# Optimization experiments

Measured on AMD Instinct MI355X. Metric: run time of the kernel, lower is better.

Reference implementation:

```python
import jax, jax.numpy as jnp
import numpy as np

B, T, D = 8, 2048, 1024
H, C, DV = 8, 64, 128   # n_heads, latent_dim, d_head
LN_EPS = 1e-5
NORM_EPS = 1e-12  # F.normalize eps


def _xavier(k, shape, fan_in, fan_out):
    lim = float(np.sqrt(6.0 / (fan_in + fan_out)))
    return jax.random.uniform(k, shape, jnp.float32, -lim, lim)


def setup_inputs() -> dict:
    key = jax.random.key(0)
    ks = jax.random.split(key, 9)
    x = jax.random.normal(ks[0], (B, T, D), jnp.float32)
    Wq = _xavier(ks[1], (C, D), D, C)            # S_q weight (out,in)
    Wk = _xavier(ks[2], (C, D), D, C)            # S_k
    Wv = _xavier(ks[3], (C, D), D, C)            # S_v
    Qc = _xavier(ks[4], (H, C, C), C, C)         # per-head latent rotations
    Vc = _xavier(ks[5], (H, C, DV), C, DV)       # per-head value up-proj
    Wa_w = _xavier(ks[6], (H * C, D), D, H * C)  # W_alpha weight
    Wa_b = jnp.full((H * C,), 3.0, jnp.float32)  # W_alpha bias init = 3.0
    Wo = _xavier(ks[7], (D, H * DV), H * DV, D)  # output proj
    gamma = jnp.ones((D,), jnp.float32)
    beta = jnp.zeros((D,), jnp.float32)
    return {"x": x, "Wq": Wq, "Wk": Wk, "Wv": Wv, "Qc": Qc, "Vc": Vc,
            "Wa_w": Wa_w, "Wa_b": Wa_b, "Wo": Wo, "gamma": gamma, "beta": beta}


def _forward(x, Wq, Wk, Wv, Qc, Vc, Wa_w, Wa_b, Wo, gamma, beta):
    residual = x
    # LayerNorm (biased variance, like torch)
    mu = jnp.mean(x, axis=-1, keepdims=True)
    var = jnp.mean(jnp.square(x - mu), axis=-1, keepdims=True)
    xn = (x - mu) * jax.lax.rsqrt(var + LN_EPS) * gamma + beta

    q_lat = xn @ Wq.T          # (B,T,C)
    k_lat = xn @ Wk.T          # (B,T,C) shared across heads
    v_lat = xn @ Wv.T          # (B,T,C)

    q = jnp.einsum('btc,hce->bhte', q_lat, Qc)   # (B,H,T,C)
    v = jnp.einsum('btc,hcd->bhtd', v_lat, Vc)   # (B,H,T,DV)
    alpha = jax.nn.sigmoid(xn @ Wa_w.T + Wa_b)   # (B,T,H*C)
    alpha = alpha.reshape(x.shape[0], x.shape[1], H, C).transpose(0, 2, 1, 3)  # (B,H,T,C)

    # F.normalize(k, dim=-1): k / max(||k||, eps)
    kn = k_lat / jnp.maximum(jnp.linalg.norm(k_lat, axis=-1, keepdims=True), NORM_EPS)

    # time-major for scan
    qs = jnp.moveaxis(q, 2, 0)      # (T,B,H,C)
    vs = jnp.moveaxis(v, 2, 0)      # (T,B,H,DV)
    als = jnp.moveaxis(alpha, 2, 0)  # (T,B,H,C)
    kns = jnp.moveaxis(kn, 1, 0)    # (T,B,C)

    S0 = jnp.zeros((x.shape[0], H, C, DV), x.dtype)

    def step(S, inp):
        q_t, k_t, v_t, a_t = inp
        # S_t = diag(alpha_t) S_{t-1} + k_t v_t^T  (k shared across heads)
        S = a_t[..., None] * S + k_t[:, None, :, None] * v_t[..., None, :]
        o_t = jnp.einsum('bhcv,bhc->bhv', S, q_t)
        return S, o_t

    _, outs = jax.lax.scan(step, S0, (qs, kns, vs, als))  # outs: (T,B,H,DV)
    out = jnp.moveaxis(outs, 0, 1).reshape(x.shape[0], x.shape[1], H * DV)
    return out @ Wo.T + residual


def reference(x, Wq, Wk, Wv, Qc, Vc, Wa_w, Wa_b, Wo, gamma, beta):
    return _forward(x, Wq, Wk, Wv, Qc, Vc, Wa_w, Wa_b, Wo, gamma, beta)
```

## Files before the change

### kernel.cpp

```cpp
#include <hip/hip_runtime.h>

typedef unsigned short u16;
typedef unsigned int   u32;
typedef __bf16 bf16x8 __attribute__((ext_vector_type(8)));
typedef float  f32x4  __attribute__((ext_vector_type(4)));
typedef float  f32x16 __attribute__((ext_vector_type(16)));

#define B_  8
#define T_  2048
#define D_  1024
#define H_  8
#define C_  64
#define DV_ 128
#define M_  (B_*T_)
#define L_  128
#define NC_ (T_/L_)
#define TS_ 8

__device__ __forceinline__ u16 f2bf(float f){
  u32 u = __float_as_uint(f);
  u32 r = (u + 0x7fffu + ((u >> 16) & 1u)) >> 16;
  return (u16)r;
}
__device__ __forceinline__ float bf2f(u16 u){
  return __uint_as_float(((u32)u) << 16);
}

__global__ __launch_bounds__(256) void ln_kernel(
    const float* __restrict__ x, const float* __restrict__ gamma,
    const float* __restrict__ beta, u16* __restrict__ xnb){
  const int m = blockIdx.x;
  const int tid = threadIdx.x;
  const int wave = tid >> 6, lane = tid & 63;
  const float* xr = x + (size_t)m * D_;
  float4 xv = *(const float4*)&xr[tid*4];
  float s = xv.x + xv.y + xv.z + xv.w;
  #pragma unroll
  for (int off = 32; off > 0; off >>= 1) s += __shfl_xor(s, off, 64);
  __shared__ float red[8];
  if (lane == 0) red[wave] = s;
  __syncthreads();
  float mu = (red[0]+red[1]+red[2]+red[3]) * (1.f/1024.f);
  float dx = xv.x-mu, dy = xv.y-mu, dz = xv.z-mu, dw = xv.w-mu;
  float ss = dx*dx + dy*dy + dz*dz + dw*dw;
  #pragma unroll
  for (int off = 32; off > 0; off >>= 1) ss += __shfl_xor(ss, off, 64);
  if (lane == 0) red[4+wave] = ss;
  __syncthreads();
  float var = (red[4]+red[5]+red[6]+red[7]) * (1.f/1024.f);
  float rs = rsqrtf(var + 1e-5f);
  float4 g  = *(const float4*)&gamma[tid*4];
  float4 bb = *(const float4*)&beta[tid*4];
  ushort4 o4;
  o4.x = f2bf(dx*rs*g.x + bb.x);
  o4.y = f2bf(dy*rs*g.y + bb.y);
  o4.z = f2bf(dz*rs*g.z + bb.z);
  o4.w = f2bf(dw*rs*g.w + bb.w);
  *(ushort4*)&xnb[(size_t)m*D_ + tid*4] = o4;
}

__global__ __launch_bounds__(256) void prep_weights(
    const float* __restrict__ Wq, const float* __restrict__ Wk,
    const float* __restrict__ Wv, const float* __restrict__ Wa,
    const float* __restrict__ Qc, const float* __restrict__ Vc,
    const float* __restrict__ Wo,
    u16* __restrict__ Wcatb, u16* __restrict__ QcTb,
    u16* __restrict__ VcTb,  u16* __restrict__ Wob){
  int idx = blockIdx.x * 256 + threadIdx.x;
  if (idx < 720896){
    int r = idx >> 10, col = idx & 1023;
    float v;
    if (r < 64)       v = Wq[(size_t)r*1024 + col];
    else if (r < 128) v = Wk[(size_t)(r-64)*1024 + col];
    else if (r < 192) v = Wv[(size_t)(r-128)*1024 + col];
    else              v = Wa[(size_t)(r-192)*1024 + col];
    Wcatb[idx] = f2bf(v);
  } else if (idx < 753664){
    int i = idx - 720896;
    int n = i >> 6, c = i & 63; int h = n >> 6, e = n & 63;
    QcTb[i] = f2bf(Qc[((size_t)h*64 + c)*64 + e]);
  } else if (idx < 819200){
    int i = idx - 753664;
    int n = i >> 6, c = i & 63; int h = n >> 7, d = n & 127;
    VcTb[i] = f2bf(Vc[((size_t)h*64 + c)*128 + d]);
  } else if (idx < 1867776){
    int i = idx - 819200;
    Wob[i] = f2bf(Wo[i]);
  }
}

__global__ __launch_bounds__(256) void gemm_bf16(
    const u16* __restrict__ A, const u16* __restrict__ Bw,
    float* __restrict__ C, const float* __restrict__ res,
    u16* __restrict__ Cb, int N, int K){
  __shared__ u16 As[128][36];
  __shared__ u16 Bs[64][36];
  const int tid = threadIdx.x;
  const int wave = tid >> 6;
  const int lane = tid & 63;
  const int q  = lane >> 4;
  const int mr = lane & 15;
  const int m0 = blockIdx.x * 128;
  const int n0 = blockIdx.y * 64;

  union FragU { u32 u[4]; bf16x8 v; };
  f32x4 zero = {0.f, 0.f, 0.f, 0.f};
  f32x4 acc[2][4];
  #pragma unroll
  for (int i = 0; i < 2; i++)
    #pragma unroll
    for (int j = 0; j < 4; j++) acc[i][j] = zero;

  for (int k0 = 0; k0 < K; k0 += 32){
    #pragma unroll
    for (int p = 0; p < 2; ++p){
      int ch = p*256 + tid;
      int r = ch >> 2, c4 = ch & 3;
      const uint4 val = *(const uint4*)(&A[(size_t)(m0 + r)*K + k0 + c4*8]);
      u32* dst = (u32*)&As[r][c4*8];
      dst[0]=val.x; dst[1]=val.y; dst[2]=val.z; dst[3]=val.w;
    }
    {
      int r = tid >> 2, c4 = tid & 3;
      const uint4 val = *(const uint4*)(&Bw[(size_t)(n0 + r)*K + k0 + c4*8]);
      u32* dst = (u32*)&Bs[r][c4*8];
      dst[0]=val.x; dst[1]=val.y; dst[2]=val.z; dst[3]=val.w;
    }
    __syncthreads();
    bf16x8 afr[2], bfr[4];
    #pragma unroll
    for (int mt = 0; mt < 2; mt++){
      const u32* p = (const u32*)&As[wave*32 + mt*16 + mr][q*8];
      FragU f; f.u[0]=p[0]; f.u[1]=p[1]; f.u[2]=p[2]; f.u[3]=p[3];
      afr[mt] = f.v;
    }
    #pragma unroll
    for (int nt = 0; nt < 4; nt++){
      const u32* p = (const u32*)&Bs[nt*16 + mr][q*8];
      FragU f; f.u[0]=p[0]; f.u[1]=p[1]; f.u[2]=p[2]; f.u[3]=p[3];
      bfr[nt] = f.v;
    }
    #pragma unroll
    for (int mt = 0; mt < 2; mt++)
      #pragma unroll
      for (int nt = 0; nt < 4; nt++)
        acc[mt][nt] = __builtin_amdgcn_mfma_f32_16x16x32_bf16(
            afr[mt], bfr[nt], acc[mt][nt], 0, 0, 0);
    __syncthreads();
  }

  #pragma unroll
  for (int mt = 0; mt < 2; mt++)
    #pragma unroll
    for (int nt = 0; nt < 4; nt++)
      #pragma unroll
      for (int r = 0; r < 4; r++){
        int row = m0 + wave*32 + mt*16 + q*4 + r;
        int col = n0 + nt*16 + mr;
        size_t idx = (size_t)row * N + col;
        float v = acc[mt][nt][r];
        if (res) v += res[idx];
        if (Cb) Cb[idx] = f2bf(v);
        else    C[idx] = v;
      }
}

__global__ __launch_bounds__(256) void split_proj(
    const float* __restrict__ proj, const float* __restrict__ Wab,
    u16* __restrict__ qlatb, float* __restrict__ knf,
    u16* __restrict__ vlatb, float* __restrict__ alphaf){
  const int m = blockIdx.x * 4 + (threadIdx.x >> 6);
  const int lane = threadIdx.x & 63;
  const float* pr = proj + (size_t)m * 704;
  qlatb[(size_t)m*64 + lane] = f2bf(pr[lane]);
  float kv = pr[64 + lane];
  float ss = kv * kv;
  #pragma unroll
  for (int off = 32; off > 0; off >>= 1) ss += __shfl_xor(ss, off, 64);
  float nrm = fmaxf(sqrtf(ss), 1e-12f);
  knf[(size_t)m*64 + lane] = kv / nrm;
  vlatb[(size_t)m*64 + lane] = f2bf(pr[128 + lane]);
  #pragma unroll
  for (int j = 0; j < 8; j++){
    int jj = j*64 + lane;
    float av = pr[192 + jj] + Wab[jj];
    alphaf[(size_t)m*512 + jj] = 1.f / (1.f + expf(-av));
  }
}


__device__ __forceinline__ void sload2(const float* ap, const float* kp,
                                       f32x16& a16, f32x16& k16){
  asm volatile("s_load_dwordx16 %0, %2, 0x0\n\t"
               "s_load_dwordx16 %1, %3, 0x0\n\t"
               "s_waitcnt lgkmcnt(0)"
               : "=&s"(a16), "=&s"(k16)
               : "s"(ap), "s"(kp));
}
__device__ __forceinline__ void sload3(const float* ap, const float* kp,
                                       const float* qp,
                                       f32x16& a16, f32x16& k16, f32x16& q16){
  asm volatile("s_load_dwordx16 %0, %3, 0x0\n\t"
               "s_load_dwordx16 %1, %4, 0x0\n\t"
               "s_load_dwordx16 %2, %5, 0x0\n\t"
               "s_waitcnt lgkmcnt(0)"
               : "=&s"(a16), "=&s"(k16), "=&s"(q16)
               : "s"(ap), "s"(kp), "s"(qp));
}

__global__ __launch_bounds__(512, 8) void scan_pass1(
    const float* __restrict__ knf, const u16* __restrict__ vb,
    const float* __restrict__ alphaf,
    float* __restrict__ Sbuf, float* __restrict__ btot){
  const int ch = blockIdx.x;
  const int bh = blockIdx.y;
  const int b = bh >> 3, h = bh & 7;
  const int tid = threadIdx.x;
  const int g = __builtin_amdgcn_readfirstlane(tid >> 7);
  const int d = tid & 127;
  const int t0 = ch * L_;

  const float* kp = knf    + ((size_t)(b*T_ + t0))*64  + g*16;
  const float* ap = alphaf + ((size_t)(b*T_ + t0))*512 + h*64 + g*16;
  const u16*   vp = vb     + ((size_t)(b*T_ + t0))*1024 + h*128 + d;

  float S[16];
  #pragma unroll
  for (int i = 0; i < 16; i++) S[i] = 0.f;
  float bt = 1.f;

  for (int t = 0; t < L_; t++){
    float vd = bf2f(vp[0]);
    float al = 1.f;
    if (d < 16) al = ap[d];
    f32x16 a16, k16;
    sload2(ap, kp, a16, k16);
    #pragma unroll
    for (int i = 0; i < 16; i++)
      S[i] = a16[i]*S[i] + k16[i]*vd;
    bt *= al;
    kp += 64; ap += 512; vp += 1024;
  }

  float* Sl = Sbuf + ((size_t)bh*NC_ + ch) * (64*128);
  #pragma unroll
  for (int i = 0; i < 16; i++) Sl[(size_t)(g*16+i)*128 + d] = S[i];
  if (d < 16) btot[((size_t)bh*NC_ + ch)*64 + g*16 + d] = bt;
}

__global__ __launch_bounds__(256) void scan_combine(
    float* __restrict__ Sbuf, const float* __restrict__ btot){
  const int bh = blockIdx.x;
  const int tid = threadIdx.x;
  float S[32];
  #pragma unroll
  for (int i = 0; i < 32; i++) S[i] = 0.f;
  float*       Sb  = Sbuf + (size_t)bh*NC_*8192;
  const float* btb = btot + (size_t)bh*NC_*64;
  for (int j = 0; j < NC_; j++){
    if (j < NC_-1){
      #pragma unroll
      for (int i = 0; i < 32; i++){
        int e = i*256 + tid;
        float loc = Sb[(size_t)j*8192 + e];
        float bv  = btb[j*64 + (e >> 7)];
        Sb[(size_t)j*8192 + e] = S[i];
        S[i] = bv * S[i] + loc;
      }
    } else {
      #pragma unroll
      for (int i = 0; i < 32; i++) Sb[(size_t)j*8192 + i*256 + tid] = S[i];
    }
  }
}

__global__ __launch_bounds__(512, 8) void scan_pass2(
    const float* __restrict__ qf, const float* __restrict__ knf,
    const u16* __restrict__ vb, const float* __restrict__ alphaf,
    const float* __restrict__ Sbuf, u16* __restrict__ ob){
  const int ch = blockIdx.x;
  const int bh = blockIdx.y;
  const int b = bh >> 3, h = bh & 7;
  const int tid = threadIdx.x;
  const int g = __builtin_amdgcn_readfirstlane(tid >> 7);
  const int d = tid & 127;
  const int t0 = ch * L_;
  __shared__ __align__(16) float sO[4][TS_][128];

  const float* qp = qf     + ((size_t)(b*T_ + t0))*512 + h*64 + g*16;
  const float* kp = knf    + ((size_t)(b*T_ + t0))*64  + g*16;
  const float* ap = alphaf + ((size_t)(b*T_ + t0))*512 + h*64 + g*16;
  const u16*   vp = vb     + ((size_t)(b*T_ + t0))*1024 + h*128 + d;
  u16*         obase = ob  + ((size_t)(b*T_ + t0))*1024 + h*128;

  float S[16];
  const float* Si = Sbuf + ((size_t)bh*NC_ + ch) * (64*128);
  #pragma unroll
  for (int i = 0; i < 16; i++) S[i] = Si[(size_t)(g*16+i)*128 + d];

  for (int sb = 0; sb < L_/TS_; sb++){
    #pragma unroll
    for (int tt = 0; tt < TS_; tt++){
      float vd = bf2f(vp[0]);
      f32x16 a16, k16, q16;
      sload3(ap, kp, qp, a16, k16, q16);
      float o0 = 0.f, o1 = 0.f, o2 = 0.f, o3 = 0.f;
      #pragma unroll
      for (int i = 0; i < 16; i += 4){
        S[i+0] = a16[i+0]*S[i+0] + k16[i+0]*vd;  o0 += S[i+0]*q16[i+0];
        S[i+1] = a16[i+1]*S[i+1] + k16[i+1]*vd;  o1 += S[i+1]*q16[i+1];
        S[i+2] = a16[i+2]*S[i+2] + k16[i+2]*vd;  o2 += S[i+2]*q16[i+2];
        S[i+3] = a16[i+3]*S[i+3] + k16[i+3]*vd;  o3 += S[i+3]*q16[i+3];
      }
      sO[g][tt][d] = (o0+o1)+(o2+o3);
      kp += 64; ap += 512; qp += 512; vp += 1024;
    }
    __syncthreads();
    #pragma unroll
    for (int i = 0; i < 2; i++){
      int idx = i*512 + tid;
      int tt = idx >> 7, dd = idx & 127;
      float o = sO[0][tt][dd] + sO[1][tt][dd] + sO[2][tt][dd] + sO[3][tt][dd];
      obase[(size_t)(sb*TS_+tt)*1024 + dd] = f2bf(o);
    }
    __syncthreads();
  }
}

extern "C" void kernel_launch(void* const* d_in, const int* in_sizes, int n_in,
                              void* d_out, int out_size, void* d_ws, size_t ws_size,
                              hipStream_t stream){
  const float* x     = (const float*)d_in[0];
  const float* Wq    = (const float*)d_in[1];
  const float* Wk    = (const float*)d_in[2];
  const float* Wv    = (const float*)d_in[3];
  const float* Qc    = (const float*)d_in[4];
  const float* Vc    = (const float*)d_in[5];
  const float* Wa_w  = (const float*)d_in[6];
  const float* Wa_b  = (const float*)d_in[7];
  const float* Wo    = (const float*)d_in[8];
  const float* gamma = (const float*)d_in[9];
  const float* beta  = (const float*)d_in[10];
  float* out = (float*)d_out;

  char* ws = (char*)d_ws;
  size_t off = 0;
  auto alloc = [&](size_t bytes) -> void* {
    void* p = ws + off; off += (bytes + 255) & ~(size_t)255; return p;
  };
  char* R1 = (char*)alloc((size_t)M_ * 1024 * 2);
  u16*   xnb  = (u16*)R1;
  u16*   obuf = (u16*)R1;
  char* R2 = (char*)alloc((size_t)M_ * 704 * 4);
  float* proj = (float*)R2;
  float* qf   = (float*)R2;
  float* Sbuf   = (float*)alloc((size_t)64 * NC_ * 8192 * 4);
  u16*   vfb    = (u16*)alloc((size_t)M_ * 1024 * 2);
  float* alphaf = (float*)alloc((size_t)M_ * 512 * 4);
  float* knf    = (float*)alloc((size_t)M_ * 64 * 4);
  u16*   qlatb  = (u16*)alloc((size_t)M_ * 64 * 2);
  u16*   vlatb  = (u16*)alloc((size_t)M_ * 64 * 2);
  u16*   Wcatb  = (u16*)alloc((size_t)704 * 1024 * 2);
  u16*   QcTb   = (u16*)alloc((size_t)512 * 64 * 2);
  u16*   VcTb   = (u16*)alloc((size_t)1024 * 64 * 2);
  u16*   Wob    = (u16*)alloc((size_t)1024 * 1024 * 2);
  float* btotp  = (float*)alloc((size_t)64 * NC_ * 64 * 4);
  (void)ws_size; (void)in_sizes; (void)n_in; (void)out_size;

  ln_kernel<<<dim3(M_), dim3(256), 0, stream>>>(x, gamma, beta, xnb);
  prep_weights<<<dim3(7296), dim3(256), 0, stream>>>(
      Wq, Wk, Wv, Wa_w, Qc, Vc, Wo, Wcatb, QcTb, VcTb, Wob);
  gemm_bf16<<<dim3(M_/128, 704/64), dim3(256), 0, stream>>>(
      xnb, Wcatb, proj, nullptr, nullptr, 704, 1024);
  split_proj<<<dim3(M_/4), dim3(256), 0, stream>>>(
      proj, Wa_b, qlatb, knf, vlatb, alphaf);
  gemm_bf16<<<dim3(M_/128, 1024/64), dim3(256), 0, stream>>>(
      vlatb, VcTb, nullptr, nullptr, vfb, 1024, 64);
  gemm_bf16<<<dim3(M_/128, 512/64), dim3(256), 0, stream>>>(
      qlatb, QcTb, qf, nullptr, nullptr, 512, 64);
  scan_pass1<<<dim3(NC_-1, 64), dim3(512), 0, stream>>>(
      knf, vfb, alphaf, Sbuf, btotp);
  scan_combine<<<dim3(64), dim3(256), 0, stream>>>(Sbuf, btotp);
  scan_pass2<<<dim3(NC_, 64), dim3(512), 0, stream>>>(
      qf, knf, vfb, alphaf, Sbuf, obuf);
  gemm_bf16<<<dim3(M_/128, 1024/64), dim3(256), 0, stream>>>(
      obuf, Wob, out, x, nullptr, 1024, 1024);
}
```

Measured before the change: 544.5 us.

## Remap scan threads to 8 waves × 2 value columns with double-buffered output reduction

Both scan passes now give each wave 8 latent rows and each lane 2 adjacent value columns, read as one packed u32 of two bf16 values, instead of 4 groups of 16 rows by 1 column. Two timesteps are processed per scalar-load batch using s_load_dwordx8 at two offsets, which halves the number of load-wait round trips per timestep. In pass2 the shared output buffer is double-buffered across sub-blocks, so one __syncthreads per 4 timesteps replaces two per 8. The reduction now sums 8 partials instead of 4, and per-lane state falls from 16 to 16 registers in a different layout.

```diff
diff --git a/kernel.cpp b/kernel.cpp
--- a/kernel.cpp
+++ b/kernel.cpp
@@ -4,7 +4,7 @@
 typedef unsigned int   u32;
 typedef __bf16 bf16x8 __attribute__((ext_vector_type(8)));
 typedef float  f32x4  __attribute__((ext_vector_type(4)));
-typedef float  f32x16 __attribute__((ext_vector_type(16)));
+typedef float  f32x8  __attribute__((ext_vector_type(8)));
 
 #define B_  8
 #define T_  2048
@@ -15,7 +15,6 @@
 #define M_  (B_*T_)
 #define L_  128
 #define NC_ (T_/L_)
-#define TS_ 8
 
 __device__ __forceinline__ u16 f2bf(float f){
   u32 u = __float_as_uint(f);
@@ -189,25 +188,6 @@
 }
 
 
-__device__ __forceinline__ void sload2(const float* ap, const float* kp,
-                                       f32x16& a16, f32x16& k16){
-  asm volatile("s_load_dwordx16 %0, %2, 0x0\n\t"
-               "s_load_dwordx16 %1, %3, 0x0\n\t"
-               "s_waitcnt lgkmcnt(0)"
-               : "=&s"(a16), "=&s"(k16)
-               : "s"(ap), "s"(kp));
-}
-__device__ __forceinline__ void sload3(const float* ap, const float* kp,
-                                       const float* qp,
-                                       f32x16& a16, f32x16& k16, f32x16& q16){
-  asm volatile("s_load_dwordx16 %0, %3, 0x0\n\t"
-               "s_load_dwordx16 %1, %4, 0x0\n\t"
-               "s_load_dwordx16 %2, %5, 0x0\n\t"
-               "s_waitcnt lgkmcnt(0)"
-               : "=&s"(a16), "=&s"(k16), "=&s"(q16)
-               : "s"(ap), "s"(kp), "s"(qp));
-}
-
 __global__ __launch_bounds__(512, 8) void scan_pass1(
     const float* __restrict__ knf, const u16* __restrict__ vb,
     const float* __restrict__ alphaf,
@@ -216,36 +196,56 @@
   const int bh = blockIdx.y;
   const int b = bh >> 3, h = bh & 7;
   const int tid = threadIdx.x;
-  const int g = __builtin_amdgcn_readfirstlane(tid >> 7);
-  const int d = tid & 127;
+  const int w = __builtin_amdgcn_readfirstlane(tid >> 6);
+  const int dg = tid & 63;
   const int t0 = ch * L_;
 
-  const float* kp = knf    + ((size_t)(b*T_ + t0))*64  + g*16;
-  const float* ap = alphaf + ((size_t)(b*T_ + t0))*512 + h*64 + g*16;
-  const u16*   vp = vb     + ((size_t)(b*T_ + t0))*1024 + h*128 + d;
-
-  float S[16];
-  #pragma unroll
-  for (int i = 0; i < 16; i++) S[i] = 0.f;
+  const float* kp  = knf    + ((size_t)(b*T_ + t0))*64  + w*8;
+  const float* ap  = alphaf + ((size_t)(b*T_ + t0))*512 + h*64 + w*8;
+  const float* alp = ap + (dg & 7);
+  const u32*   vp  = (const u32*)(vb + ((size_t)(b*T_ + t0))*1024 + h*128) + dg;
+
+  float S[8][2];
+  #pragma unroll
+  for (int j = 0; j < 8; j++){ S[j][0] = 0.f; S[j][1] = 0.f; }
   float bt = 1.f;
 
-  for (int t = 0; t < L_; t++){
-    float vd = bf2f(vp[0]);
-    float al = 1.f;
-    if (d < 16) al = ap[d];
-    f32x16 a16, k16;
-    sload2(ap, kp, a16, k16);
-    #pragma unroll
-    for (int i = 0; i < 16; i++)
-      S[i] = a16[i]*S[i] + k16[i]*vd;
-    bt *= al;
-    kp += 64; ap += 512; vp += 1024;
+  for (int t = 0; t < L_; t += 2){
+    f32x8 a0, a1, k0, k1;
+    asm volatile(
+      "s_load_dwordx8 %0, %4, 0x0\n\t"
+      "s_load_dwordx8 %1, %4, 0x800\n\t"
+      "s_load_dwordx8 %2, %5, 0x0\n\t"
+      "s_load_dwordx8 %3, %5, 0x100\n\t"
+      "s_waitcnt lgkmcnt(0)"
+      : "=&s"(a0), "=&s"(a1), "=&s"(k0), "=&s"(k1)
+      : "s"(ap), "s"(kp));
+    float al0 = alp[0], al1 = alp[512];
+    u32 vv0 = vp[0], vv1 = vp[512];
+    float v00 = __uint_as_float(vv0 << 16);
+    float v01 = __uint_as_float(vv0 & 0xffff0000u);
+    float v10 = __uint_as_float(vv1 << 16);
+    float v11 = __uint_as_float(vv1 & 0xffff0000u);
+    #pragma unroll
+    for (int j = 0; j < 8; j++){
+      S[j][0] = a0[j]*S[j][0] + k0[j]*v00;
+      S[j][1] = a0[j]*S[j][1] + k0[j]*v01;
+    }
+    bt *= al0;
+    #pragma unroll
+    for (int j = 0; j < 8; j++){
+      S[j][0] = a1[j]*S[j][0] + k1[j]*v10;
+      S[j][1] = a1[j]*S[j][1] + k1[j]*v11;
+    }
+    bt *= al1;
+    ap += 1024; kp += 128; alp += 1024; vp += 1024;
   }
 
   float* Sl = Sbuf + ((size_t)bh*NC_ + ch) * (64*128);
   #pragma unroll
-  for (int i = 0; i < 16; i++) Sl[(size_t)(g*16+i)*128 + d] = S[i];
-  if (d < 16) btot[((size_t)bh*NC_ + ch)*64 + g*16 + d] = bt;
+  for (int j = 0; j < 8; j++)
+    *(float2*)&Sl[(size_t)(w*8+j)*128 + 2*dg] = make_float2(S[j][0], S[j][1]);
+  if (dg < 8) btot[((size_t)bh*NC_ + ch)*64 + w*8 + dg] = bt;
 }
 
 __global__ __launch_bounds__(256) void scan_combine(
@@ -282,48 +282,85 @@
   const int bh = blockIdx.y;
   const int b = bh >> 3, h = bh & 7;
   const int tid = threadIdx.x;
-  const int g = __builtin_amdgcn_readfirstlane(tid >> 7);
-  const int d = tid & 127;
+  const int w = __builtin_amdgcn_readfirstlane(tid >> 6);
+  const int dg = tid & 63;
   const int t0 = ch * L_;
-  __shared__ __align__(16) float sO[4][TS_][128];
-
-  const float* qp = qf     + ((size_t)(b*T_ + t0))*512 + h*64 + g*16;
-  const float* kp = knf    + ((size_t)(b*T_ + t0))*64  + g*16;
-  const float* ap = alphaf + ((size_t)(b*T_ + t0))*512 + h*64 + g*16;
-  const u16*   vp = vb     + ((size_t)(b*T_ + t0))*1024 + h*128 + d;
-  u16*         obase = ob  + ((size_t)(b*T_ + t0))*1024 + h*128;
-
-  float S[16];
+  __shared__ __align__(16) float sO[2][8][4][128];
+
+  const float* qp = qf     + ((size_t)(b*T_ + t0))*512 + h*64 + w*8;
+  const float* kp = knf    + ((size_t)(b*T_ + t0))*64  + w*8;
+  const float* ap = alphaf + ((size_t)(b*T_ + t0))*512 + h*64 + w*8;
+  const u32*   vp = (const u32*)(vb + ((size_t)(b*T_ + t0))*1024 + h*128) + dg;
+  u16* obase = ob + ((size_t)(b*T_ + t0))*1024 + h*128;
+
+  float S[8][2];
   const float* Si = Sbuf + ((size_t)bh*NC_ + ch) * (64*128);
   #pragma unroll
-  for (int i = 0; i < 16; i++) S[i] = Si[(size_t)(g*16+i)*128 + d];
-
-  for (int sb = 0; sb < L_/TS_; sb++){
-    #pragma unroll
-    for (int tt = 0; tt < TS_; tt++){
-      float vd = bf2f(vp[0]);
-      f32x16 a16, k16, q16;
-      sload3(ap, kp, qp, a16, k16, q16);
-      float o0 = 0.f, o1 = 0.f, o2 = 0.f, o3 = 0.f;
-      #pragma unroll
-      for (int i = 0; i < 16; i += 4){
-        S[i+0] = a16[i+0]*S[i+0] + k16[i+0]*vd;  o0 += S[i+0]*q16[i+0];
-        S[i+1] = a16[i+1]*S[i+1] + k16[i+1]*vd;  o1 += S[i+1]*q16[i+1];
-        S[i+2] = a16[i+2]*S[i+2] + k16[i+2]*vd;  o2 += S[i+2]*q16[i+2];
-        S[i+3] = a16[i+3]*S[i+3] + k16[i+3]*vd;  o3 += S[i+3]*q16[i+3];
+  for (int j = 0; j < 8; j++){
+    float2 s2 = *(const float2*)&Si[(size_t)(w*8+j)*128 + 2*dg];
+    S[j][0] = s2.x; S[j][1] = s2.y;
+  }
+
+  const int rtt = tid >> 7, rdd = tid & 127;
+
+  for (int sb = 0; sb < L_/4; sb++){
+    const int p = sb & 1;
+    #pragma unroll
+    for (int half = 0; half < 2; half++){
+      f32x8 a0, a1, k0, k1, q0, q1;
+      asm volatile(
+        "s_load_dwordx8 %0, %6, 0x0\n\t"
+        "s_load_dwordx8 %1, %6, 0x800\n\t"
+        "s_load_dwordx8 %2, %7, 0x0\n\t"
+        "s_load_dwordx8 %3, %7, 0x100\n\t"
+        "s_load_dwordx8 %4, %8, 0x0\n\t"
+        "s_load_dwordx8 %5, %8, 0x800\n\t"
+        "s_waitcnt lgkmcnt(0)"
+        : "=&s"(a0), "=&s"(a1), "=&s"(k0), "=&s"(k1), "=&s"(q0), "=&s"(q1)
+        : "s"(ap), "s"(kp), "s"(qp));
+      u32 vv0 = vp[0], vv1 = vp[512];
+      float v00 = __uint_as_float(vv0 << 16);
+      float v01 = __uint_as_float(vv0 & 0xffff0000u);
+      float v10 = __uint_as_float(vv1 << 16);
+      float v11 = __uint_as_float(vv1 & 0xffff0000u);
+      {
+        float oa0, oa1, ob0, ob1;
+        S[0][0] = a0[0]*S[0][0] + k0[0]*v00;  oa0 = S[0][0]*q0[0];
+        S[0][1] = a0[0]*S[0][1] + k0[0]*v01;  oa1 = S[0][1]*q0[0];
+        S[1][0] = a0[1]*S[1][0] + k0[1]*v00;  ob0 = S[1][0]*q0[1];
+        S[1][1] = a0[1]*S[1][1] + k0[1]*v01;  ob1 = S[1][1]*q0[1];
+        #pragma unroll
+        for (int j = 2; j < 8; j += 2){
+          S[j][0]   = a0[j]*S[j][0]     + k0[j]*v00;    oa0 += S[j][0]*q0[j];
+          S[j][1]   = a0[j]*S[j][1]     + k0[j]*v01;    oa1 += S[j][1]*q0[j];
+          S[j+1][0] = a0[j+1]*S[j+1][0] + k0[j+1]*v00;  ob0 += S[j+1][0]*q0[j+1];
+          S[j+1][1] = a0[j+1]*S[j+1][1] + k0[j+1]*v01;  ob1 += S[j+1][1]*q0[j+1];
+        }
+        *(float2*)&sO[p][w][half*2+0][2*dg] = make_float2(oa0+ob0, oa1+ob1);
       }
-      sO[g][tt][d] = (o0+o1)+(o2+o3);
-      kp += 64; ap += 512; qp += 512; vp += 1024;
+      {
+        float oa0, oa1, ob0, ob1;
+        S[0][0] = a1[0]*S[0][0] + k1[0]*v10;  oa0 = S[0][0]*q1[0];
+        S[0][1] = a1[0]*S[0][1] + k1[0]*v11;  oa1 = S[0][1]*q1[0];
+        S[1][0] = a1[1]*S[1][0] + k1[1]*v10;  ob0 = S[1][0]*q1[1];
+        S[1][1] = a1[1]*S[1][1] + k1[1]*v11;  ob1 = S[1][1]*q1[1];
+        #pragma unroll
+        for (int j = 2; j < 8; j += 2){
+          S[j][0]   = a1[j]*S[j][0]     + k1[j]*v10;    oa0 += S[j][0]*q1[j];
+          S[j][1]   = a1[j]*S[j][1]     + k1[j]*v11;    oa1 += S[j][1]*q1[j];
+          S[j+1][0] = a1[j+1]*S[j+1][0] + k1[j+1]*v10;  ob0 += S[j+1][0]*q1[j+1];
+          S[j+1][1] = a1[j+1]*S[j+1][1] + k1[j+1]*v11;  ob1 += S[j+1][1]*q1[j+1];
+        }
+        *(float2*)&sO[p][w][half*2+1][2*dg] = make_float2(oa0+ob0, oa1+ob1);
+      }
+      ap += 1024; kp += 128; qp += 1024; vp += 1024;
     }
     __syncthreads();
-    #pragma unroll
-    for (int i = 0; i < 2; i++){
-      int idx = i*512 + tid;
-      int tt = idx >> 7, dd = idx & 127;
-      float o = sO[0][tt][dd] + sO[1][tt][dd] + sO[2][tt][dd] + sO[3][tt][dd];
-      obase[(size_t)(sb*TS_+tt)*1024 + dd] = f2bf(o);
-    }
-    __syncthreads();
+    float o = sO[p][0][rtt][rdd] + sO[p][1][rtt][rdd]
+            + sO[p][2][rtt][rdd] + sO[p][3][rtt][rdd]
+            + sO[p][4][rtt][rdd] + sO[p][5][rtt][rdd]
+            + sO[p][6][rtt][rdd] + sO[p][7][rtt][rdd];
+    obase[(size_t)(sb*4 + rtt)*1024 + rdd] = f2bf(o);
   }
 }
 
```

New measurement: 538.9 us. Within noise of the previous version (-1.0%).
